# Optimization experiments

Measured on AMD Instinct MI355X. Metric: run time of the kernel, lower is better.

## Reference

```python
import jax, jax.numpy as jnp
import numpy as np


def setup_inputs() -> dict:
    key = jax.random.key(0)
    k1, k2, k3, k4 = jax.random.split(key, 4)
    P, BPP, S, DIN, DOUT, LEVELS = 8, 8, 4096, 256, 256, 7  # parscale_n, batch/path, seq, dims, bit levels (2..8)
    x = jax.random.normal(k1, (P * BPP, S, DIN), dtype=jnp.float32)
    # one dequantized weight per bit level (stand-in for mp_weight.get_weight(bits))
    weight_bank = jax.random.normal(k2, (LEVELS, DOUT, DIN), dtype=jnp.float32) * 0.02
    bias = jax.random.normal(k3, (DOUT,), dtype=jnp.float32) * 0.02
    assigned_bits = jax.random.randint(k4, (P,), 0, LEVELS, dtype=jnp.int64)  # index into weight_bank
    return {"x": x, "weight_bank": weight_bank, "bias": bias, "assigned_bits": assigned_bits}


def reference(x, weight_bank, bias, assigned_bits):
    P = assigned_bits.shape[0]
    B, S, Din = x.shape
    bpp = B // P
    xs = x.reshape(P, bpp, S, Din)                 # [P, bpp, S, Din]
    W = weight_bank[assigned_bits]                 # per-path weight select [P, Dout, Din]
    out = jnp.einsum('pbsi,poi->pbso', xs, W) + bias  # grouped dequant-matmul
    return out.reshape(P * bpp, S, -1)
```

## Files before the change

kernel.cpp:

```cpp
#include <hip/hip_runtime.h>


typedef float  floatx4  __attribute__((ext_vector_type(4)));
typedef short  shortx8  __attribute__((ext_vector_type(8)));
typedef unsigned short ushortx4 __attribute__((ext_vector_type(4)));

constexpr int DIN  = 256;
constexpr int DOUT = 256;
constexpr int ROWS_PER_PATH = 8 * 4096;
constexpr int BM   = 32;
constexpr int WBANK_ELEMS = 7 * DOUT * DIN;

__device__ __forceinline__ unsigned short f2bf(float f) {
  union { float f; unsigned u; } c; c.f = f;
  unsigned r = c.u + 0x7fffu + ((c.u >> 16) & 1u);
  return (unsigned short)(r >> 16);
}

__device__ __forceinline__ shortx8 cvt8(floatx4 v0, floatx4 v1) {
  shortx8 h;
  h[0] = (short)f2bf(v0.x); h[1] = (short)f2bf(v0.y);
  h[2] = (short)f2bf(v0.z); h[3] = (short)f2bf(v0.w);
  h[4] = (short)f2bf(v1.x); h[5] = (short)f2bf(v1.y);
  h[6] = (short)f2bf(v1.z); h[7] = (short)f2bf(v1.w);
  return h;
}

__global__ void convert_w_kernel(const float* __restrict__ w,
                                 unsigned short* __restrict__ o, int n4) {
  int i = blockIdx.x * 256 + threadIdx.x;
  if (i < n4) {
    floatx4 v = ((const floatx4*)w)[i];
    ushortx4 h;
    h.x = f2bf(v.x); h.y = f2bf(v.y); h.z = f2bf(v.z); h.w = f2bf(v.w);
    ((ushortx4*)o)[i] = h;
  }
}

template <bool WBF>
__global__ __launch_bounds__(256, 2)
void mp_linear_kernel(const float* __restrict__ x,
                      const void*  __restrict__ wsel,
                      const float* __restrict__ bias,
                      const int*   __restrict__ bits,
                      float* __restrict__ out) {
  __shared__ short xs[BM * DIN];

  const int tid  = threadIdx.x;
  const int row0 = blockIdx.x * BM;
  const int path = row0 / ROWS_PER_PATH;
  const int widx = bits[path];

  const int lane = tid & 63;
  const int wave = tid >> 6;
  const int n0   = wave * 64;
  const int quad = lane >> 4;
  const int l16  = lane & 15;

  const float* xt = x + (size_t)row0 * DIN;
  floatx4 v[8];
#pragma unroll
  for (int c = 0; c < 4; ++c) {
    const float* p = xt + (size_t)(tid + c * 256) * 8;
    v[2 * c]     = *(const floatx4*)p;
    v[2 * c + 1] = *(const floatx4*)(p + 4);
  }

  shortx8 w[4][8];
  if (WBF) {
    const unsigned short* __restrict__ wp =
        (const unsigned short*)wsel + (size_t)widx * (DOUT * DIN)
        + (size_t)(n0 + l16) * DIN + quad * 8;
#pragma unroll
    for (int nf = 0; nf < 4; ++nf)
#pragma unroll
      for (int kk = 0; kk < 8; ++kk)
        w[nf][kk] = *(const shortx8*)(wp + (size_t)(nf * 16) * DIN + kk * 32);
  } else {
    const float* __restrict__ wp =
        (const float*)wsel + (size_t)widx * (DOUT * DIN)
        + (size_t)(n0 + l16) * DIN + quad * 8;
#pragma unroll
    for (int nf = 0; nf < 4; ++nf)
#pragma unroll
      for (int kk = 0; kk < 8; ++kk) {
        const float* p = wp + (size_t)(nf * 16) * DIN + kk * 32;
        w[nf][kk] = cvt8(*(const floatx4*)p, *(const floatx4*)(p + 4));
      }
  }

#pragma unroll
  for (int c = 0; c < 4; ++c) {
    const int g   = tid + c * 256;
    const int row = g >> 5;
    const int col = (g & 31) * 8;
    int byte = (row * DIN + col) * 2;
    byte ^= (row & 7) << 4;
    *(shortx8*)((char*)xs + byte) = cvt8(v[2 * c], v[2 * c + 1]);
  }
  __syncthreads();

  floatx4 acc[2][4];
#pragma unroll
  for (int i = 0; i < 2; ++i)
#pragma unroll
    for (int j = 0; j < 4; ++j)
      acc[i][j] = (floatx4)0.f;

#pragma unroll
  for (int kk = 0; kk < 8; ++kk) {
    const int k0 = kk * 32;
    shortx8 xf[2];
#pragma unroll
    for (int mf = 0; mf < 2; ++mf) {
      const int row = mf * 16 + l16;
      int byte = (row * DIN + k0 + quad * 8) * 2;
      byte ^= (row & 7) << 4;
      xf[mf] = *(const shortx8*)((const char*)xs + byte);
    }
#pragma unroll
    for (int mf = 0; mf < 2; ++mf)
#pragma unroll
      for (int nf = 0; nf < 4; ++nf)
        acc[mf][nf] = __builtin_amdgcn_mfma_f32_16x16x32_bf16(
            w[nf][kk], xf[mf], acc[mf][nf], 0, 0, 0);
  }

  floatx4 bv[4];
#pragma unroll
  for (int nf = 0; nf < 4; ++nf)
    bv[nf] = *(const floatx4*)(bias + n0 + nf * 16 + quad * 4);

#pragma unroll
  for (int mf = 0; mf < 2; ++mf) {
    float* orow = out + (size_t)(row0 + mf * 16 + l16) * DOUT + n0 + quad * 4;
#pragma unroll
    for (int nf = 0; nf < 4; ++nf) {
      floatx4 o4 = acc[mf][nf] + bv[nf];
      __builtin_nontemporal_store(o4, (floatx4*)(orow + nf * 16));
    }
  }
}

extern "C" void kernel_launch(void* const* d_in, const int* in_sizes, int n_in,
                              void* d_out, int out_size, void* d_ws, size_t ws_size,
                              hipStream_t stream) {
  const float* x     = (const float*)d_in[0];
  const float* wbank = (const float*)d_in[1];
  const float* bias  = (const float*)d_in[2];
  const int*   bits  = (const int*)d_in[3];
  float*       out   = (float*)d_out;

  const int total_rows = in_sizes[0] / DIN;
  const int grid = total_rows / BM;

  const size_t wbf_bytes = (size_t)WBANK_ELEMS * sizeof(unsigned short);
  if (ws_size >= wbf_bytes) {
    unsigned short* wbf = (unsigned short*)d_ws;
    const int n4 = WBANK_ELEMS / 4;
    convert_w_kernel<<<(n4 + 255) / 256, 256, 0, stream>>>(wbank, wbf, n4);
    mp_linear_kernel<true><<<grid, 256, 0, stream>>>(x, wbf, bias, bits, out);
  } else {
    mp_linear_kernel<false><<<grid, 256, 0, stream>>>(x, wbank, bias, bits, out);
  }
}
```

Baseline: 513.7 us.

## Make kernel persistent per path with double-buffered async LDS staging of x

Launches a fixed 64 blocks per path instead of one block per 32-row tile. Each block keeps its path's bf16 weight fragments in registers and loops over many tiles. The next fp32 x tile is copied directly into a swizzled double-buffered LDS area with global_load_lds, overlapping the copy with the MFMA work and output stores of the current tile. The aim is to remove the per-tile weight reload and the global-load latency exposed on every tile. In exchange, LDS per block doubles to 64KB of fp32, the bf16 conversion moves into the inner loop, stores are no longer nontemporal, and correctness depends on hand-placed vmcnt waits.

```diff
diff --git a/kernel.cpp b/kernel.cpp
--- a/kernel.cpp
+++ b/kernel.cpp
@@ -7,9 +7,10 @@
 
 constexpr int DIN  = 256;
 constexpr int DOUT = 256;
-constexpr int ROWS_PER_PATH = 8 * 4096;
-constexpr int BM   = 32;
-constexpr int WBANK_ELEMS = 7 * DOUT * DIN;
+constexpr int ROWS_PER_PATH   = 8 * 4096;
+constexpr int BM              = 32;
+constexpr int BLOCKS_PER_PATH = 64;
+constexpr int WBANK_ELEMS     = 7 * DOUT * DIN;
 
 __device__ __forceinline__ unsigned short f2bf(float f) {
   union { float f; unsigned u; } c; c.f = f;
@@ -44,42 +45,31 @@
                       const float* __restrict__ bias,
                       const int*   __restrict__ bits,
                       float* __restrict__ out) {
-  __shared__ short xs[BM * DIN];
+  __shared__ float xs[2][BM * DIN];
 
   const int tid  = threadIdx.x;
-  const int row0 = blockIdx.x * BM;
-  const int path = row0 / ROWS_PER_PATH;
-  const int widx = bits[path];
-
   const int lane = tid & 63;
   const int wave = tid >> 6;
-  const int n0   = wave * 64;
   const int quad = lane >> 4;
   const int l16  = lane & 15;
+  const int n0   = wave * 64;
 
-  const float* xt = x + (size_t)row0 * DIN;
-  floatx4 v[8];
-#pragma unroll
-  for (int c = 0; c < 4; ++c) {
-    const float* p = xt + (size_t)(tid + c * 256) * 8;
-    v[2 * c]     = *(const floatx4*)p;
-    v[2 * c + 1] = *(const floatx4*)(p + 4);
-  }
+  const int path  = blockIdx.x & 7;
+  const int bslot = blockIdx.x >> 3;
+  const int widx  = bits[path];
 
   shortx8 w[4][8];
   if (WBF) {
-    const unsigned short* __restrict__ wp =
-        (const unsigned short*)wsel + (size_t)widx * (DOUT * DIN)
-        + (size_t)(n0 + l16) * DIN + quad * 8;
+    const unsigned short* wp = (const unsigned short*)wsel
+        + (size_t)widx * (DOUT * DIN) + (size_t)(n0 + l16) * DIN + quad * 8;
 #pragma unroll
     for (int nf = 0; nf < 4; ++nf)
 #pragma unroll
       for (int kk = 0; kk < 8; ++kk)
         w[nf][kk] = *(const shortx8*)(wp + (size_t)(nf * 16) * DIN + kk * 32);
   } else {
-    const float* __restrict__ wp =
-        (const float*)wsel + (size_t)widx * (DOUT * DIN)
-        + (size_t)(n0 + l16) * DIN + quad * 8;
+    const float* wp = (const float*)wsel
+        + (size_t)widx * (DOUT * DIN) + (size_t)(n0 + l16) * DIN + quad * 8;
 #pragma unroll
     for (int nf = 0; nf < 4; ++nf)
 #pragma unroll
@@ -89,56 +79,81 @@
       }
   }
 
-#pragma unroll
-  for (int c = 0; c < 4; ++c) {
-    const int g   = tid + c * 256;
-    const int row = g >> 5;
-    const int col = (g & 31) * 8;
-    int byte = (row * DIN + col) * 2;
-    byte ^= (row & 7) << 4;
-    *(shortx8*)((char*)xs + byte) = cvt8(v[2 * c], v[2 * c + 1]);
-  }
-  __syncthreads();
-
-  floatx4 acc[2][4];
-#pragma unroll
-  for (int i = 0; i < 2; ++i)
-#pragma unroll
-    for (int j = 0; j < 4; ++j)
-      acc[i][j] = (floatx4)0.f;
-
-#pragma unroll
-  for (int kk = 0; kk < 8; ++kk) {
-    const int k0 = kk * 32;
-    shortx8 xf[2];
-#pragma unroll
-    for (int mf = 0; mf < 2; ++mf) {
-      const int row = mf * 16 + l16;
-      int byte = (row * DIN + k0 + quad * 8) * 2;
-      byte ^= (row & 7) << 4;
-      xf[mf] = *(const shortx8*)((const char*)xs + byte);
-    }
-#pragma unroll
-    for (int mf = 0; mf < 2; ++mf)
-#pragma unroll
-      for (int nf = 0; nf < 4; ++nf)
-        acc[mf][nf] = __builtin_amdgcn_mfma_f32_16x16x32_bf16(
-            w[nf][kk], xf[mf], acc[mf][nf], 0, 0, 0);
-  }
-
   floatx4 bv[4];
 #pragma unroll
   for (int nf = 0; nf < 4; ++nf)
     bv[nf] = *(const floatx4*)(bias + n0 + nf * 16 + quad * 4);
 
+  const int row_base = path * ROWS_PER_PATH;
+  const int TILES    = ROWS_PER_PATH / BM;
+
+  auto stage = [&](int buf, int trow0) {
+    const char* xb = (const char*)(x + (size_t)trow0 * DIN);
 #pragma unroll
-  for (int mf = 0; mf < 2; ++mf) {
-    float* orow = out + (size_t)(row0 + mf * 16 + l16) * DOUT + n0 + quad * 4;
+    for (int i = 0; i < 8; ++i) {
+      const int row = wave * 8 + i;
+      const int swz = (row & 15) << 4;
+      const char* g = xb + (size_t)row * 1024 + ((lane * 16) ^ swz);
+      __builtin_amdgcn_global_load_lds(
+          (const __attribute__((address_space(1))) void*)g,
+          (__attribute__((address_space(3))) void*)(&xs[buf][row * 256]),
+          16, 0, 0);
+    }
+  };
+
+  int t = bslot;
+  stage(0, row_base + t * BM);
+  asm volatile("s_waitcnt vmcnt(0)" ::: "memory");
+  __builtin_amdgcn_s_barrier();
+
+  int cur = 0;
+  for (; t < TILES; t += BLOCKS_PER_PATH) {
+    const int tn = t + BLOCKS_PER_PATH;
+    const bool has_next = tn < TILES;
+    if (has_next) stage(cur ^ 1, row_base + tn * BM);
+
+    floatx4 acc[2][4];
 #pragma unroll
-    for (int nf = 0; nf < 4; ++nf) {
-      floatx4 o4 = acc[mf][nf] + bv[nf];
-      __builtin_nontemporal_store(o4, (floatx4*)(orow + nf * 16));
+    for (int i = 0; i < 2; ++i)
+#pragma unroll
+      for (int j = 0; j < 4; ++j)
+        acc[i][j] = (floatx4)0.f;
+
+    const char* bufc = (const char*)&xs[cur][0];
+#pragma unroll
+    for (int kk = 0; kk < 8; ++kk) {
+      shortx8 xf[2];
+#pragma unroll
+      for (int mf = 0; mf < 2; ++mf) {
+        const int row = mf * 16 + l16;
+        const int swz = (row & 15) << 4;
+        const int off = row * 1024 + kk * 128 + quad * 32;
+        floatx4 f0 = *(const floatx4*)(bufc + (off ^ swz));
+        floatx4 f1 = *(const floatx4*)(bufc + ((off + 16) ^ swz));
+        xf[mf] = cvt8(f0, f1);
+      }
+#pragma unroll
+      for (int mf = 0; mf < 2; ++mf)
+#pragma unroll
+        for (int nf = 0; nf < 4; ++nf)
+          acc[mf][nf] = __builtin_amdgcn_mfma_f32_16x16x32_bf16(
+              w[nf][kk], xf[mf], acc[mf][nf], 0, 0, 0);
     }
+
+    const int row0t = row_base + t * BM;
+#pragma unroll
+    for (int mf = 0; mf < 2; ++mf) {
+      float* orow = out + (size_t)(row0t + mf * 16 + l16) * DOUT + n0 + quad * 4;
+#pragma unroll
+      for (int nf = 0; nf < 4; ++nf)
+        *(floatx4*)(orow + nf * 16) = acc[mf][nf] + bv[nf];
+    }
+
+    if (has_next) {
+      asm volatile("s_waitcnt vmcnt(8)" ::: "memory");
+    }
+    __builtin_amdgcn_s_barrier();
+    cur ^= 1;
   }
 }
 
@@ -152,7 +167,8 @@
   float*       out   = (float*)d_out;
 
   const int total_rows = in_sizes[0] / DIN;
-  const int grid = total_rows / BM;
+  const int P = total_rows / ROWS_PER_PATH;
+  const int grid = P * BLOCKS_PER_PATH;
 
   const size_t wbf_bytes = (size_t)WBANK_ELEMS * sizeof(unsigned short);
   if (ws_size >= wbf_bytes) {
```

Measured after the change: 450.4 us. 12.3% less time.
